# Optimization experiments

Hardware: AMD Instinct MI355X
Metric: run time of the kernel (lower is better)

## Reference

```python
import jax, jax.numpy as jnp
import numpy as np

N = 1500                 # number of proposals
NUM_CLASSES = 81         # COCO: background + 80
NMS_THRESH = 0.5
SCORE_THRESH = 0.05
MAX_DET = 100            # config.test.max_det
BBOX_REG_WEIGHTS = jnp.array([10.0, 10.0, 5.0, 5.0], dtype=jnp.float32)


def setup_inputs() -> dict:
    key = jax.random.key(0)
    k1, k2, k3 = jax.random.split(key, 3)
    H, W = 800.0, 1333.0
    # realistic proposals: random centers / sizes inside the image
    cx = jax.random.uniform(jax.random.fold_in(k1, 0), (N,)) * W
    cy = jax.random.uniform(jax.random.fold_in(k1, 1), (N,)) * H
    bw = jax.random.uniform(jax.random.fold_in(k1, 2), (N,)) * 200.0 + 16.0
    bh = jax.random.uniform(jax.random.fold_in(k1, 3), (N,)) * 200.0 + 16.0
    bottom_rois = jnp.stack(
        [jnp.zeros((N,)), cx - 0.5 * bw, cy - 0.5 * bh, cx + 0.5 * bw, cy + 0.5 * bh],
        axis=1).astype(jnp.float32)
    bbox_delta = (jax.random.normal(k2, (N, 4 * NUM_CLASSES)) * 0.5).astype(jnp.float32)
    cls_prob = jax.nn.softmax(jax.random.normal(k3, (N, NUM_CLASSES)) * 2.0, axis=-1).astype(jnp.float32)
    im_info = jnp.array([[H, W, 1.0]], dtype=jnp.float32)
    return {"bottom_rois": bottom_rois, "bbox_delta": bbox_delta,
            "cls_prob": cls_prob, "im_info": im_info}


def _decode_boxes(rois, deltas, im_info):
    # rois [N,4], deltas [N,4C] -> clipped boxes [N,C,4] (legacy +1 convention)
    x1, y1, x2, y2 = rois[:, 0], rois[:, 1], rois[:, 2], rois[:, 3]
    w = x2 - x1 + 1.0
    h = y2 - y1 + 1.0
    cx = x1 + 0.5 * w
    cy = y1 + 0.5 * h
    d = deltas.reshape(deltas.shape[0], -1, 4) / BBOX_REG_WEIGHTS  # [N,C,4]
    pcx = cx[:, None] + w[:, None] * d[..., 0]
    pcy = cy[:, None] + h[:, None] * d[..., 1]
    pw = w[:, None] * jnp.exp(d[..., 2])
    ph = h[:, None] * jnp.exp(d[..., 3])
    boxes = jnp.stack([pcx - 0.5 * pw, pcy - 0.5 * ph,
                       pcx + 0.5 * pw - 1.0, pcy + 0.5 * ph - 1.0], axis=-1)
    hw = im_info[0, :2]  # [height, width]
    lim = jnp.stack([hw[1] - 1.0, hw[0] - 1.0, hw[1] - 1.0, hw[0] - 1.0])
    return jnp.clip(boxes, 0.0, lim)


def _pairwise_iou(b):
    # b [N,4], legacy +1 areas (matches gpu_nms)
    x1, y1, x2, y2 = b[:, 0], b[:, 1], b[:, 2], b[:, 3]
    area = (x2 - x1 + 1.0) * (y2 - y1 + 1.0)
    iw = jnp.maximum(jnp.minimum(x2[:, None], x2[None, :]) - jnp.maximum(x1[:, None], x1[None, :]) + 1.0, 0.0)
    ih = jnp.maximum(jnp.minimum(y2[:, None], y2[None, :]) - jnp.maximum(y1[:, None], y1[None, :]) + 1.0, 0.0)
    inter = iw * ih
    return inter / (area[:, None] + area[None, :] - inter)


def _nms_one_class(boxes, scores):
    # boxes [N,4], scores [N] -> score-sorted boxes/scores + keep mask
    valid = scores > SCORE_THRESH
    order = jnp.argsort(-scores)
    b = boxes[order]
    s = scores[order]
    v = valid[order]
    iou = jax.lax.stop_gradient(_pairwise_iou(b))  # used only in comparisons

    def body(suppressed, i):
        keep_i = v[i] & ~suppressed[i]
        suppressed = suppressed | (keep_i & (iou[i] > NMS_THRESH))
        return suppressed, keep_i

    _, keep = jax.lax.scan(body, jnp.zeros((b.shape[0],), bool), jnp.arange(b.shape[0]))
    return b, s, keep


def reference(bottom_rois, bbox_delta, cls_prob, im_info):
    boxes = _decode_boxes(bottom_rois[:, 1:], bbox_delta, im_info)  # [N,C,4]
    C = cls_prob.shape[1]
    boxes_fg = jnp.swapaxes(boxes, 0, 1)[1:]   # [C-1,N,4]
    scores_fg = cls_prob.T[1:]                 # [C-1,N]
    b, s, keep = jax.vmap(_nms_one_class)(boxes_fg, scores_fg)
    # image-level max_det cap (>= kth score, as in source)
    flat = jnp.where(keep, s, -jnp.inf).reshape(-1)
    n_keep = keep.sum()
    kth = jax.lax.top_k(flat, MAX_DET)[0][-1]
    keep = keep & jnp.where(n_keep > MAX_DET, s >= kth, True)
    cls_idx = jnp.broadcast_to(jnp.arange(1, C)[:, None], s.shape)
    zeros = jnp.zeros_like(s[..., None])
    dets = jnp.concatenate([zeros, b, s[..., None]], axis=-1)  # [C-1,N,6]
    dets = jnp.where(keep[..., None], dets, 0.0).reshape(-1, 6)
    return dets, cls_idx.reshape(-1), keep.reshape(-1)
```

## Files before the change

### kernel.cpp

```cpp
#include <hip/hip_runtime.h>
#include <math.h>

#pragma clang fp contract(off)

#define N_ROIS     1500
#define NUM_CLS    81
#define FG         80
#define MAXC       1536
#define NMS_T      0.5f
#define SCORE_T    0.05f
#define MAX_DET    100
#define TOTAL      (FG * N_ROIS)
#define TPB        256
#define NCHUNK     ((N_ROIS + TPB - 1) / TPB)

__device__ __forceinline__ unsigned f2s(float f) {
    unsigned u = __float_as_uint(f);
    return (u & 0x80000000u) ? ~u : (u | 0x80000000u);
}
__device__ __forceinline__ float s2f(unsigned u) {
    return __uint_as_float((u & 0x80000000u) ? (u & 0x7FFFFFFFu) : ~u);
}

__global__ __launch_bounds__(TPB) void nms_fused(
    const float* __restrict__ rois,
    const float* __restrict__ deltas,
    const float* __restrict__ prob,
    const float* __restrict__ iminfo,
    float4* __restrict__ keptBox,
    int*    __restrict__ keptRow,
    float*  __restrict__ keptScore,
    int*    __restrict__ ctrs,
    float*  __restrict__ out)
{
    __shared__ unsigned long long key[MAXC];
    __shared__ unsigned long long skey[MAXC];
    __shared__ float4 box4[MAXC];
    __shared__ float  areaA[MAXC];
    __shared__ unsigned char keepf[MAXC], supp[MAXC];
    __shared__ int hist[256];
    __shared__ int wtot[4];
    __shared__ unsigned s_pref;
    __shared__ int s_kk;
    __shared__ int mcnt, s_arr;

    const int tid  = threadIdx.x;
    const int lane = tid & 63;
    const int wv   = tid >> 6;
    const int c = blockIdx.x + 1;
    const int cbase = blockIdx.x * N_ROIS;

    if (tid == 0) mcnt = 0;
    __syncthreads();

    float sv[NCHUNK];
    #pragma unroll
    for (int t = 0; t < NCHUNK; ++t) {
        int i = t * TPB + tid;
        sv[t] = (i < N_ROIS) ? prob[i * NUM_CLS + c] : 0.0f;
    }
    #pragma unroll
    for (int t = 0; t < NCHUNK; ++t) {
        int i = t * TPB + tid;
        bool val = (i < N_ROIS) && (sv[t] > SCORE_T);
        unsigned long long m = __ballot(val);
        int base = 0;
        if (lane == 0 && m) base = atomicAdd(&mcnt, __popcll(m));
        base = __shfl(base, 0, 64);
        if (val) {
            int pos = base + __popcll(m & ((1ull << lane) - 1ull));
            key[pos] = ((unsigned long long)(~f2s(sv[t])) << 32) | (unsigned)i;
        }
    }

    {
        const float4 z4 = make_float4(0.f, 0.f, 0.f, 0.f);
        float4* dets4 = (float4*)(out + (size_t)cbase * 6);
        for (int i = tid; i < N_ROIS * 6 / 4; i += TPB) dets4[i] = z4;
        const float fc = (float)c;
        const float4 c4 = make_float4(fc, fc, fc, fc);
        float4* cls4  = (float4*)(out + (size_t)TOTAL * 6 + cbase);
        float4* keep4 = (float4*)(out + (size_t)TOTAL * 7 + cbase);
        for (int i = tid; i < N_ROIS / 4; i += TPB) { cls4[i] = c4; keep4[i] = z4; }
    }
    __syncthreads();
    const int M = mcnt;

    if (M > 0) {
        for (int i = tid; i < M; i += TPB) {
            unsigned long long kk = key[i];
            int cnt = 0;
            #pragma unroll 4
            for (int j = 0; j < M; ++j) cnt += (int)(key[j] < kk);
            skey[cnt] = kk;
        }
        __syncthreads();

        const float Hm1 = iminfo[0] - 1.0f;
        const float Wm1 = iminfo[1] - 1.0f;
        for (int k = tid; k < M; k += TPB) {
            unsigned long long kk = skey[k];
            int i = (int)(kk & 0xFFFFFFFFu);
            const float* rp = rois + i * 5;
            float x1 = rp[1], y1 = rp[2], x2 = rp[3], y2 = rp[4];
            float w  = x2 - x1 + 1.0f;
            float h  = y2 - y1 + 1.0f;
            float cx = x1 + 0.5f * w;
            float cy = y1 + 0.5f * h;
            const float* dp = deltas + i * (4 * NUM_CLS) + c * 4;
            float dx = dp[0] / 10.0f, dy = dp[1] / 10.0f;
            float dw = dp[2] / 5.0f,  dh = dp[3] / 5.0f;
            float pcx = cx + w * dx;
            float pcy = cy + h * dy;
            float pw  = w * expf(dw);
            float ph  = h * expf(dh);
            float a1 = pcx - 0.5f * pw;
            float a2 = pcy - 0.5f * ph;
            float a3 = pcx + 0.5f * pw - 1.0f;
            float a4 = pcy + 0.5f * ph - 1.0f;
            a1 = fminf(fmaxf(a1, 0.0f), Wm1);
            a2 = fminf(fmaxf(a2, 0.0f), Hm1);
            a3 = fminf(fmaxf(a3, 0.0f), Wm1);
            a4 = fminf(fmaxf(a4, 0.0f), Hm1);
            box4[k]  = make_float4(a1, a2, a3, a4);
            areaA[k] = (a3 - a1 + 1.0f) * (a4 - a2 + 1.0f);
            keepf[k] = 0; supp[k] = 0;
        }
        __syncthreads();

        const int MW = (M + 63) >> 6;
        const bool fast = (M * MW <= MAXC);

        if (fast) {
            for (int r = wv; r < M; r += TPB / 64) {
                float4 br = box4[r];
                float  ar = areaA[r];
                for (int w = 0; w < MW; ++w) {
                    int col = (w << 6) | lane;
                    bool inb = (col < M);
                    int j = inb ? col : 0;
                    float4 bj = box4[j];
                    float  aj = areaA[j];
                    float iw = fminf(br.z, bj.z) - fmaxf(br.x, bj.x) + 1.0f;
                    float ih = fminf(br.w, bj.w) - fmaxf(br.y, bj.y) + 1.0f;
                    iw = fmaxf(iw, 0.0f);
                    ih = fmaxf(ih, 0.0f);
                    float inter = iw * ih;
                    float iou = inter / ((ar + aj) - inter);
                    bool pred = inb && (col > r) && (iou > NMS_T);
                    unsigned long long mk = __ballot(pred);
                    if (lane == 0) key[r * MW + w] = mk;
                }
            }
            __syncthreads();

            if (tid < 64) {
                const int lw = (tid < MW) ? tid : 0;
                unsigned long long acc = 0;
                unsigned long long mcur = key[lw];
                for (int k = 0; k < M; ++k) {
                    unsigned long long mnext =
                        (k + 1 < M) ? key[(k + 1) * MW + lw] : 0ull;
                    int bit = (int)((acc >> (k & 63)) & 1ull);
                    int sup = __shfl(bit, k >> 6, 64);
                    if (!sup) {
                        acc |= mcur;
                        if (tid == 0) keepf[k] = 1;
                    }
                    mcur = mnext;
                }
            }
            __syncthreads();
        } else {
            for (int k = 0; k < M; ++k) {
                if (!supp[k]) {
                    if (tid == 0) keepf[k] = 1;
                    float4 bk = box4[k];
                    float  ak = areaA[k];
                    for (int j = k + 1 + tid; j < M; j += TPB) {
                        float4 bj = box4[j];
                        float  aj = areaA[j];
                        float iw = fminf(bk.z, bj.z) - fmaxf(bk.x, bj.x) + 1.0f;
                        float ih = fminf(bk.w, bj.w) - fmaxf(bk.y, bj.y) + 1.0f;
                        iw = fmaxf(iw, 0.0f);
                        ih = fmaxf(ih, 0.0f);
                        float inter = iw * ih;
                        float iou = inter / ((ak + aj) - inter);
                        if (iou > NMS_T) supp[j] = 1;
                    }
                }
                __syncthreads();
            }
        }

        for (int k = tid; k < M; k += TPB) {
            if (keepf[k]) {
                int p = atomicAdd(&ctrs[0], 1);
                keptRow[p]   = cbase + k;
                keptBox[p]   = box4[k];
                keptScore[p] = s2f(~(unsigned)(skey[k] >> 32));
            }
        }
    }

    __threadfence();
    if (tid == 0) s_arr = atomicAdd(&ctrs[1], 1);
    __syncthreads();
    if (s_arr != FG - 1) return;
    __threadfence();

    const int n = ctrs[0];
    const bool filt = (n > MAX_DET);
    float kth = -INFINITY;

    if (filt) {
        if (tid == 0) { s_pref = 0u; s_kk = MAX_DET; }
        __syncthreads();
        for (int d = 0; d < 4; ++d) {
            const int shift = 24 - 8 * d;
            hist[tid] = 0;
            __syncthreads();
            const unsigned pref = s_pref;
            for (int i = tid; i < n; i += TPB) {
                unsigned u = f2s(keptScore[i]);
                if (d == 0 || (u >> (shift + 8)) == pref)
                    atomicAdd(&hist[(u >> shift) & 255u], 1);
            }
            __syncthreads();
            const int h = hist[tid];
            int r = h;
            #pragma unroll
            for (int off = 1; off < 64; off <<= 1) {
                int o = __shfl_down(r, off, 64);
                if (lane + off < 64) r += o;
            }
            if (lane == 0) wtot[wv] = r;
            __syncthreads();
            int hi = 0;
            #pragma unroll
            for (int w2 = 0; w2 < 4; ++w2) if (w2 > wv) hi += wtot[w2];
            const int S_ge = r + hi;
            const int S_gt = S_ge - h;
            const int kk = s_kk;
            if (S_gt < kk && S_ge >= kk) {
                s_pref = (pref << 8) | (unsigned)tid;
                s_kk   = kk - S_gt;
            }
            __syncthreads();
        }
        kth = s2f(s_pref);
    }

    for (int i = tid; i < n; i += TPB) {
        float s = keptScore[i];
        if (!filt || s >= kth) {
            int r = keptRow[i];
            float4 b4 = keptBox[i];
            float* dst = out + (size_t)r * 6;
            dst[1] = b4.x; dst[2] = b4.y; dst[3] = b4.z; dst[4] = b4.w; dst[5] = s;
            out[(size_t)TOTAL * 7 + r] = 1.0f;
        }
    }
}

extern "C" void kernel_launch(void* const* d_in, const int* in_sizes, int n_in,
                              void* d_out, int out_size, void* d_ws, size_t ws_size,
                              hipStream_t stream) {
    const float* rois   = (const float*)d_in[0];
    const float* deltas = (const float*)d_in[1];
    const float* prob   = (const float*)d_in[2];
    const float* iminfo = (const float*)d_in[3];
    float* out = (float*)d_out;

    float4* keptBox   = (float4*)d_ws;
    int*    keptRow   = (int*)(keptBox + TOTAL);
    float*  keptScore = (float*)(keptRow + TOTAL);
    int*    ctrs      = (int*)(keptScore + TOTAL);

    hipMemsetAsync(ctrs, 0, 2 * sizeof(int), stream);
    nms_fused<<<FG, TPB, 0, stream>>>(rois, deltas, prob, iminfo,
                                      keptBox, keptRow, keptScore, ctrs, out);
}
```

Measured before the change: 117.8 us.

## Split fused NMS into per-class, kth-select, fill and patch kernels

The single fused kernel is replaced by four launches. The first does per-class NMS only, and it skips IoU work for the mask words below the diagonal by writing zeros to them. A dedicated single-block kernel finds the kth score using per-wave histograms and compacts the matching candidates into LDS. A grid-wide fill kernel then zeroes the outputs, and a multi-block patch kernel scatters the kept detections. This drops the last-block-arrives serial tail and the per-class output zeroing inside the NMS blocks, at the cost of extra kernel launch overhead and a dependent launch chain.

```diff
diff --git a/kernel.cpp b/kernel.cpp
--- a/kernel.cpp
+++ b/kernel.cpp
@@ -13,6 +13,7 @@
 #define TOTAL      (FG * N_ROIS)
 #define TPB        256
 #define NCHUNK     ((N_ROIS + TPB - 1) / TPB)
+#define SUBCAP     8192
 
 __device__ __forceinline__ unsigned f2s(float f) {
     unsigned u = __float_as_uint(f);
@@ -22,7 +23,7 @@
     return __uint_as_float((u & 0x80000000u) ? (u & 0x7FFFFFFFu) : ~u);
 }
 
-__global__ __launch_bounds__(TPB) void nms_fused(
+__global__ __launch_bounds__(TPB) void nms_k1(
     const float* __restrict__ rois,
     const float* __restrict__ deltas,
     const float* __restrict__ prob,
@@ -30,19 +31,14 @@
     float4* __restrict__ keptBox,
     int*    __restrict__ keptRow,
     float*  __restrict__ keptScore,
-    int*    __restrict__ ctrs,
-    float*  __restrict__ out)
+    int*    __restrict__ ctrs)
 {
     __shared__ unsigned long long key[MAXC];
     __shared__ unsigned long long skey[MAXC];
     __shared__ float4 box4[MAXC];
     __shared__ float  areaA[MAXC];
     __shared__ unsigned char keepf[MAXC], supp[MAXC];
-    __shared__ int hist[256];
-    __shared__ int wtot[4];
-    __shared__ unsigned s_pref;
-    __shared__ int s_kk;
-    __shared__ int mcnt, s_arr;
+    __shared__ int mcnt;
 
     const int tid  = threadIdx.x;
     const int lane = tid & 63;
@@ -72,188 +68,272 @@
             key[pos] = ((unsigned long long)(~f2s(sv[t])) << 32) | (unsigned)i;
         }
     }
-
-    {
-        const float4 z4 = make_float4(0.f, 0.f, 0.f, 0.f);
-        float4* dets4 = (float4*)(out + (size_t)cbase * 6);
-        for (int i = tid; i < N_ROIS * 6 / 4; i += TPB) dets4[i] = z4;
-        const float fc = (float)c;
-        const float4 c4 = make_float4(fc, fc, fc, fc);
-        float4* cls4  = (float4*)(out + (size_t)TOTAL * 6 + cbase);
-        float4* keep4 = (float4*)(out + (size_t)TOTAL * 7 + cbase);
-        for (int i = tid; i < N_ROIS / 4; i += TPB) { cls4[i] = c4; keep4[i] = z4; }
-    }
     __syncthreads();
     const int M = mcnt;
-
-    if (M > 0) {
-        for (int i = tid; i < M; i += TPB) {
-            unsigned long long kk = key[i];
-            int cnt = 0;
-            #pragma unroll 4
-            for (int j = 0; j < M; ++j) cnt += (int)(key[j] < kk);
-            skey[cnt] = kk;
-        }
-        __syncthreads();
-
-        const float Hm1 = iminfo[0] - 1.0f;
-        const float Wm1 = iminfo[1] - 1.0f;
-        for (int k = tid; k < M; k += TPB) {
-            unsigned long long kk = skey[k];
-            int i = (int)(kk & 0xFFFFFFFFu);
-            const float* rp = rois + i * 5;
-            float x1 = rp[1], y1 = rp[2], x2 = rp[3], y2 = rp[4];
-            float w  = x2 - x1 + 1.0f;
-            float h  = y2 - y1 + 1.0f;
-            float cx = x1 + 0.5f * w;
-            float cy = y1 + 0.5f * h;
-            const float* dp = deltas + i * (4 * NUM_CLS) + c * 4;
-            float dx = dp[0] / 10.0f, dy = dp[1] / 10.0f;
-            float dw = dp[2] / 5.0f,  dh = dp[3] / 5.0f;
-            float pcx = cx + w * dx;
-            float pcy = cy + h * dy;
-            float pw  = w * expf(dw);
-            float ph  = h * expf(dh);
-            float a1 = pcx - 0.5f * pw;
-            float a2 = pcy - 0.5f * ph;
-            float a3 = pcx + 0.5f * pw - 1.0f;
-            float a4 = pcy + 0.5f * ph - 1.0f;
-            a1 = fminf(fmaxf(a1, 0.0f), Wm1);
-            a2 = fminf(fmaxf(a2, 0.0f), Hm1);
-            a3 = fminf(fmaxf(a3, 0.0f), Wm1);
-            a4 = fminf(fmaxf(a4, 0.0f), Hm1);
-            box4[k]  = make_float4(a1, a2, a3, a4);
-            areaA[k] = (a3 - a1 + 1.0f) * (a4 - a2 + 1.0f);
-            keepf[k] = 0; supp[k] = 0;
-        }
-        __syncthreads();
-
-        const int MW = (M + 63) >> 6;
-        const bool fast = (M * MW <= MAXC);
-
-        if (fast) {
-            for (int r = wv; r < M; r += TPB / 64) {
-                float4 br = box4[r];
-                float  ar = areaA[r];
-                for (int w = 0; w < MW; ++w) {
-                    int col = (w << 6) | lane;
-                    bool inb = (col < M);
-                    int j = inb ? col : 0;
+    if (M == 0) return;
+
+    for (int i = tid; i < M; i += TPB) {
+        unsigned long long kk = key[i];
+        int cnt = 0;
+        #pragma unroll 4
+        for (int j = 0; j < M; ++j) cnt += (int)(key[j] < kk);
+        skey[cnt] = kk;
+    }
+    __syncthreads();
+
+    const float Hm1 = iminfo[0] - 1.0f;
+    const float Wm1 = iminfo[1] - 1.0f;
+    for (int k = tid; k < M; k += TPB) {
+        unsigned long long kk = skey[k];
+        int i = (int)(kk & 0xFFFFFFFFu);
+        const float* rp = rois + i * 5;
+        float x1 = rp[1], y1 = rp[2], x2 = rp[3], y2 = rp[4];
+        float w  = x2 - x1 + 1.0f;
+        float h  = y2 - y1 + 1.0f;
+        float cx = x1 + 0.5f * w;
+        float cy = y1 + 0.5f * h;
+        const float* dp = deltas + i * (4 * NUM_CLS) + c * 4;
+        float dx = dp[0] / 10.0f, dy = dp[1] / 10.0f;
+        float dw = dp[2] / 5.0f,  dh = dp[3] / 5.0f;
+        float pcx = cx + w * dx;
+        float pcy = cy + h * dy;
+        float pw  = w * expf(dw);
+        float ph  = h * expf(dh);
+        float a1 = pcx - 0.5f * pw;
+        float a2 = pcy - 0.5f * ph;
+        float a3 = pcx + 0.5f * pw - 1.0f;
+        float a4 = pcy + 0.5f * ph - 1.0f;
+        a1 = fminf(fmaxf(a1, 0.0f), Wm1);
+        a2 = fminf(fmaxf(a2, 0.0f), Hm1);
+        a3 = fminf(fmaxf(a3, 0.0f), Wm1);
+        a4 = fminf(fmaxf(a4, 0.0f), Hm1);
+        box4[k]  = make_float4(a1, a2, a3, a4);
+        areaA[k] = (a3 - a1 + 1.0f) * (a4 - a2 + 1.0f);
+        keepf[k] = 0; supp[k] = 0;
+    }
+    __syncthreads();
+
+    const int MW = (M + 63) >> 6;
+    const bool fast = (M * MW <= MAXC);
+
+    if (fast) {
+        for (int r = wv; r < M; r += TPB / 64) {
+            float4 br = box4[r];
+            float  ar = areaA[r];
+            const int w0 = r >> 6;
+            if (lane == 0)
+                for (int w = 0; w < w0; ++w) key[r * MW + w] = 0ull;
+            for (int w = w0; w < MW; ++w) {
+                int col = (w << 6) | lane;
+                bool inb = (col < M);
+                int j = inb ? col : 0;
+                float4 bj = box4[j];
+                float  aj = areaA[j];
+                float iw = fminf(br.z, bj.z) - fmaxf(br.x, bj.x) + 1.0f;
+                float ih = fminf(br.w, bj.w) - fmaxf(br.y, bj.y) + 1.0f;
+                iw = fmaxf(iw, 0.0f);
+                ih = fmaxf(ih, 0.0f);
+                float inter = iw * ih;
+                float iou = inter / ((ar + aj) - inter);
+                bool pred = inb && (col > r) && (iou > NMS_T);
+                unsigned long long mk = __ballot(pred);
+                if (lane == 0) key[r * MW + w] = mk;
+            }
+        }
+        __syncthreads();
+
+        if (tid < 64) {
+            const int lw = (tid < MW) ? tid : 0;
+            unsigned long long acc = 0;
+            unsigned long long mcur = key[lw];
+            for (int k = 0; k < M; ++k) {
+                unsigned long long mnext =
+                    (k + 1 < M) ? key[(k + 1) * MW + lw] : 0ull;
+                int bit = (int)((acc >> (k & 63)) & 1ull);
+                int sup = __shfl(bit, k >> 6, 64);
+                if (!sup) {
+                    acc |= mcur;
+                    if (tid == 0) keepf[k] = 1;
+                }
+                mcur = mnext;
+            }
+        }
+        __syncthreads();
+    } else {
+        for (int k = 0; k < M; ++k) {
+            if (!supp[k]) {
+                if (tid == 0) keepf[k] = 1;
+                float4 bk = box4[k];
+                float  ak = areaA[k];
+                for (int j = k + 1 + tid; j < M; j += TPB) {
                     float4 bj = box4[j];
                     float  aj = areaA[j];
-                    float iw = fminf(br.z, bj.z) - fmaxf(br.x, bj.x) + 1.0f;
-                    float ih = fminf(br.w, bj.w) - fmaxf(br.y, bj.y) + 1.0f;
+                    float iw = fminf(bk.z, bj.z) - fmaxf(bk.x, bj.x) + 1.0f;
+                    float ih = fminf(bk.w, bj.w) - fmaxf(bk.y, bj.y) + 1.0f;
                     iw = fmaxf(iw, 0.0f);
                     ih = fmaxf(ih, 0.0f);
                     float inter = iw * ih;
-                    float iou = inter / ((ar + aj) - inter);
-                    bool pred = inb && (col > r) && (iou > NMS_T);
-                    unsigned long long mk = __ballot(pred);
-                    if (lane == 0) key[r * MW + w] = mk;
+                    float iou = inter / ((ak + aj) - inter);
+                    if (iou > NMS_T) supp[j] = 1;
                 }
             }
             __syncthreads();
-
-            if (tid < 64) {
-                const int lw = (tid < MW) ? tid : 0;
-                unsigned long long acc = 0;
-                unsigned long long mcur = key[lw];
-                for (int k = 0; k < M; ++k) {
-                    unsigned long long mnext =
-                        (k + 1 < M) ? key[(k + 1) * MW + lw] : 0ull;
-                    int bit = (int)((acc >> (k & 63)) & 1ull);
-                    int sup = __shfl(bit, k >> 6, 64);
-                    if (!sup) {
-                        acc |= mcur;
-                        if (tid == 0) keepf[k] = 1;
-                    }
-                    mcur = mnext;
-                }
+        }
+    }
+
+    for (int k = tid; k < M; k += TPB) {
+        if (keepf[k]) {
+            int p = atomicAdd(&ctrs[0], 1);
+            keptRow[p]   = cbase + k;
+            keptBox[p]   = box4[k];
+            keptScore[p] = s2f(~(unsigned)(skey[k] >> 32));
+        }
+    }
+}
+
+__global__ __launch_bounds__(TPB) void kth_k2(
+    const int*   __restrict__ ctrs,
+    const float* __restrict__ keptScore,
+    float* __restrict__ kth_out)
+{
+    __shared__ int hist4[4][256];
+    __shared__ unsigned sub[SUBCAP];
+    __shared__ int wtot[4];
+    __shared__ unsigned s_d0;
+    __shared__ unsigned s_sp;
+    __shared__ int s_kk, s_cnt;
+
+    const int tid  = threadIdx.x;
+    const int lane = tid & 63;
+    const int wv   = tid >> 6;
+    const int n = ctrs[0];
+
+    if (n <= MAX_DET) {
+        if (tid == 0) *kth_out = -INFINITY;
+        return;
+    }
+
+    #pragma unroll
+    for (int w = 0; w < 4; ++w) hist4[w][tid] = 0;
+    __syncthreads();
+    for (int i = tid; i < n; i += TPB)
+        atomicAdd(&hist4[wv][f2s(keptScore[i]) >> 24], 1);
+    __syncthreads();
+    {
+        const int h = hist4[0][tid] + hist4[1][tid] + hist4[2][tid] + hist4[3][tid];
+        int r = h;
+        #pragma unroll
+        for (int off = 1; off < 64; off <<= 1) {
+            int o = __shfl_down(r, off, 64);
+            if (lane + off < 64) r += o;
+        }
+        if (lane == 0) wtot[wv] = r;
+        __syncthreads();
+        int hi = 0;
+        #pragma unroll
+        for (int w2 = 0; w2 < 4; ++w2) if (w2 > wv) hi += wtot[w2];
+        const int S_ge = r + hi, S_gt = S_ge - h;
+        if (S_gt < MAX_DET && S_ge >= MAX_DET) {
+            s_d0 = (unsigned)tid;
+            s_kk = MAX_DET - S_gt;
+        }
+    }
+    if (tid == 0) { s_cnt = 0; s_sp = 0u; }
+    __syncthreads();
+    const unsigned d0 = s_d0;
+
+    for (int i0 = 0; i0 < n; i0 += TPB) {
+        int i = i0 + tid;
+        unsigned u = (i < n) ? f2s(keptScore[i]) : 0u;
+        bool match = (i < n) && ((u >> 24) == d0);
+        unsigned long long m = __ballot(match);
+        int base = 0;
+        if (lane == 0 && m) base = atomicAdd(&s_cnt, __popcll(m));
+        base = __shfl(base, 0, 64);
+        if (match) {
+            int pos = base + __popcll(m & ((1ull << lane) - 1ull));
+            if (pos < SUBCAP) sub[pos] = u & 0xFFFFFFu;
+        }
+    }
+    __syncthreads();
+    const int ns = s_cnt;
+    const bool inLds = (ns <= SUBCAP);
+    const int limit = inLds ? ns : n;
+
+    for (int d = 1; d < 4; ++d) {
+        const int shift = 24 - 8 * d;
+        #pragma unroll
+        for (int w = 0; w < 4; ++w) hist4[w][tid] = 0;
+        __syncthreads();
+        const unsigned sp = s_sp;
+        for (int i = tid; i < limit; i += TPB) {
+            unsigned v; bool ok;
+            if (inLds) { v = sub[i]; ok = true; }
+            else {
+                unsigned u = f2s(keptScore[i]);
+                ok = ((u >> 24) == d0);
+                v = u & 0xFFFFFFu;
             }
-            __syncthreads();
-        } else {
-            for (int k = 0; k < M; ++k) {
-                if (!supp[k]) {
-                    if (tid == 0) keepf[k] = 1;
-                    float4 bk = box4[k];
-                    float  ak = areaA[k];
-                    for (int j = k + 1 + tid; j < M; j += TPB) {
-                        float4 bj = box4[j];
-                        float  aj = areaA[j];
-                        float iw = fminf(bk.z, bj.z) - fmaxf(bk.x, bj.x) + 1.0f;
-                        float ih = fminf(bk.w, bj.w) - fmaxf(bk.y, bj.y) + 1.0f;
-                        iw = fmaxf(iw, 0.0f);
-                        ih = fmaxf(ih, 0.0f);
-                        float inter = iw * ih;
-                        float iou = inter / ((ak + aj) - inter);
-                        if (iou > NMS_T) supp[j] = 1;
-                    }
-                }
-                __syncthreads();
-            }
-        }
-
-        for (int k = tid; k < M; k += TPB) {
-            if (keepf[k]) {
-                int p = atomicAdd(&ctrs[0], 1);
-                keptRow[p]   = cbase + k;
-                keptBox[p]   = box4[k];
-                keptScore[p] = s2f(~(unsigned)(skey[k] >> 32));
-            }
-        }
-    }
-
-    __threadfence();
-    if (tid == 0) s_arr = atomicAdd(&ctrs[1], 1);
-    __syncthreads();
-    if (s_arr != FG - 1) return;
-    __threadfence();
-
+            if (ok && (d == 1 || (v >> (shift + 8)) == sp))
+                atomicAdd(&hist4[wv][(v >> shift) & 255u], 1);
+        }
+        __syncthreads();
+        const int h = hist4[0][tid] + hist4[1][tid] + hist4[2][tid] + hist4[3][tid];
+        int r = h;
+        #pragma unroll
+        for (int off = 1; off < 64; off <<= 1) {
+            int o = __shfl_down(r, off, 64);
+            if (lane + off < 64) r += o;
+        }
+        if (lane == 0) wtot[wv] = r;
+        __syncthreads();
+        int hi = 0;
+        #pragma unroll
+        for (int w2 = 0; w2 < 4; ++w2) if (w2 > wv) hi += wtot[w2];
+        const int S_ge = r + hi, S_gt = S_ge - h;
+        const int kk = s_kk;
+        if (S_gt < kk && S_ge >= kk) {
+            s_sp = (s_sp << 8) | (unsigned)tid;
+            s_kk = kk - S_gt;
+        }
+        __syncthreads();
+    }
+
+    if (tid == 0) *kth_out = s2f((d0 << 24) | s_sp);
+}
+
+__global__ __launch_bounds__(TPB) void fill_k3(float* __restrict__ out)
+{
+    const float4 z4 = make_float4(0.f, 0.f, 0.f, 0.f);
+    const int stride = gridDim.x * TPB;
+    int g = blockIdx.x * TPB + threadIdx.x;
+
+    float4* dets4 = (float4*)out;
+    for (int i = g; i < TOTAL * 6 / 4; i += stride) dets4[i] = z4;
+
+    float4* cls4  = (float4*)(out + (size_t)TOTAL * 6);
+    float4* keep4 = (float4*)(out + (size_t)TOTAL * 7);
+    for (int i = g; i < TOTAL / 4; i += stride) {
+        float fc = (float)((i * 4) / N_ROIS + 1);
+        cls4[i]  = make_float4(fc, fc, fc, fc);
+        keep4[i] = z4;
+    }
+}
+
+__global__ __launch_bounds__(TPB) void patch_k4(
+    const int*    __restrict__ ctrs,
+    const int*    __restrict__ keptRow,
+    const float4* __restrict__ keptBox,
+    const float*  __restrict__ keptScore,
+    const float*  __restrict__ kth_ptr,
+    float* __restrict__ out)
+{
     const int n = ctrs[0];
-    const bool filt = (n > MAX_DET);
-    float kth = -INFINITY;
-
-    if (filt) {
-        if (tid == 0) { s_pref = 0u; s_kk = MAX_DET; }
-        __syncthreads();
-        for (int d = 0; d < 4; ++d) {
-            const int shift = 24 - 8 * d;
-            hist[tid] = 0;
-            __syncthreads();
-            const unsigned pref = s_pref;
-            for (int i = tid; i < n; i += TPB) {
-                unsigned u = f2s(keptScore[i]);
-                if (d == 0 || (u >> (shift + 8)) == pref)
-                    atomicAdd(&hist[(u >> shift) & 255u], 1);
-            }
-            __syncthreads();
-            const int h = hist[tid];
-            int r = h;
-            #pragma unroll
-            for (int off = 1; off < 64; off <<= 1) {
-                int o = __shfl_down(r, off, 64);
-                if (lane + off < 64) r += o;
-            }
-            if (lane == 0) wtot[wv] = r;
-            __syncthreads();
-            int hi = 0;
-            #pragma unroll
-            for (int w2 = 0; w2 < 4; ++w2) if (w2 > wv) hi += wtot[w2];
-            const int S_ge = r + hi;
-            const int S_gt = S_ge - h;
-            const int kk = s_kk;
-            if (S_gt < kk && S_ge >= kk) {
-                s_pref = (pref << 8) | (unsigned)tid;
-                s_kk   = kk - S_gt;
-            }
-            __syncthreads();
-        }
-        kth = s2f(s_pref);
-    }
-
-    for (int i = tid; i < n; i += TPB) {
+    const float kth = *kth_ptr;
+    const int stride = gridDim.x * TPB;
+    for (int i = blockIdx.x * TPB + threadIdx.x; i < n; i += stride) {
         float s = keptScore[i];
-        if (!filt || s >= kth) {
+        if (s >= kth) {
             int r = keptRow[i];
             float4 b4 = keptBox[i];
             float* dst = out + (size_t)r * 6;
@@ -276,8 +356,12 @@
     int*    keptRow   = (int*)(keptBox + TOTAL);
     float*  keptScore = (float*)(keptRow + TOTAL);
     int*    ctrs      = (int*)(keptScore + TOTAL);
-
-    hipMemsetAsync(ctrs, 0, 2 * sizeof(int), stream);
-    nms_fused<<<FG, TPB, 0, stream>>>(rois, deltas, prob, iminfo,
-                                      keptBox, keptRow, keptScore, ctrs, out);
-}
+    float*  kth       = (float*)(ctrs + 4);
+
+    hipMemsetAsync(ctrs, 0, sizeof(int), stream);
+    nms_k1<<<FG, TPB, 0, stream>>>(rois, deltas, prob, iminfo,
+                                   keptBox, keptRow, keptScore, ctrs);
+    kth_k2<<<1, TPB, 0, stream>>>(ctrs, keptScore, kth);
+    fill_k3<<<256, TPB, 0, stream>>>(out);
+    patch_k4<<<64, TPB, 0, stream>>>(ctrs, keptRow, keptBox, keptScore, kth, out);
+}
```

Result: faster. 109.5 us (-7.0%).
